# Kernel optimization log

Measured on AMD Instinct MI355X. Metric: run time of the kernel, lower is better.

The kernel has to match this reference:

```python
import jax, jax.numpy as jnp
import numpy as np
from jax import lax

T, N, E, B = 8, 50000, 100000, 512
DN = DE = DG = 128


def _linear_params(key, d_in, d_out):
    k1, k2 = jax.random.split(key)
    s = 1.0 / float(np.sqrt(d_in))
    W = jax.random.uniform(k1, (d_in, d_out), minval=-s, maxval=s, dtype=jnp.float32)
    b = jax.random.uniform(k2, (d_out,), minval=-s, maxval=s, dtype=jnp.float32)
    return W, b


def setup_inputs() -> dict:
    key = jax.random.key(0)
    ks = jax.random.split(key, 12)
    inp = {
        "xs": jax.random.normal(ks[0], (T, N, DN), dtype=jnp.float32),
        "es": jax.random.normal(ks[1], (T, E, DE), dtype=jnp.float32),
        "gs": jax.random.normal(ks[2], (T, B, DG), dtype=jnp.float32),
    }
    i = 3
    for name, d in (("node", DN), ("edge", DE), ("glob", DG)):
        W1, b1 = _linear_params(ks[i], 2 * d, d)  # sig1 sees cat(prev_out, x_t)
        W2, b2 = _linear_params(ks[i + 1], d, d)
        W3, b3 = _linear_params(ks[i + 2], d, d)
        i += 3
        inp[f"W1_{name}"], inp[f"b1_{name}"] = W1, b1
        inp[f"W2_{name}"], inp[f"b2_{name}"] = W2, b2
        inp[f"W3_{name}"], inp[f"b3_{name}"] = W3, b3
    return inp


def _run_component(seq, W1, b1, W2, b2, W3, b3):
    # seq: [T, M, d]; recurrent LSTM-style gating per element, fused in a scan.
    def step(carry, x_t):
        state, out = carry
        forget = jax.nn.sigmoid(jnp.concatenate([out, x_t], axis=-1) @ W1 + b1)
        state = state * forget + jax.nn.sigmoid(x_t @ W2 + b2) * jnp.tanh(x_t)
        out = jnp.tanh(state) * jax.nn.sigmoid(x_t @ W3 + b3)
        return (state, out), None

    (state, out), _ = lax.scan(step, (seq[0], seq[0]), seq)
    return state, out


def reference(xs, es, gs,
              W1_node, b1_node, W2_node, b2_node, W3_node, b3_node,
              W1_edge, b1_edge, W2_edge, b2_edge, W3_edge, b3_edge,
              W1_glob, b1_glob, W2_glob, b2_glob, W3_glob, b3_glob):
    sx, ox = _run_component(xs, W1_node, b1_node, W2_node, b2_node, W3_node, b3_node)
    se, oe = _run_component(es, W1_edge, b1_edge, W2_edge, b2_edge, W3_edge, b3_edge)
    sg, og = _run_component(gs, W1_glob, b1_glob, W2_glob, b2_glob, W3_glob, b3_glob)
    # (state, data) per component: node, edge, glob
    return (sx, se, sg, ox, oe, og)
```

## Files before the change

### kernel.cpp

```cpp
#include <hip/hip_runtime.h>

typedef __attribute__((ext_vector_type(8))) short bf16x8;
typedef __attribute__((ext_vector_type(4))) float f32x4;
typedef __attribute__((ext_vector_type(4))) short s16x4;

__device__ __forceinline__ unsigned cvt_pk(float lo, float hi) {
  unsigned r;
  asm("v_cvt_pk_bf16_f32 %0, %1, %2" : "=v"(r) : "v"(lo), "v"(hi));
  return r;
}
__device__ __forceinline__ float bf2f(short s) {
  return __uint_as_float(((unsigned)(unsigned short)s) << 16);
}
__device__ __forceinline__ float sigm(float z) {
  return __builtin_amdgcn_rcpf(1.f + __builtin_amdgcn_exp2f(-1.44269504089f * z));
}
__device__ __forceinline__ float tanh_(float z) {
  return 1.f - 2.f * __builtin_amdgcn_rcpf(1.f + __builtin_amdgcn_exp2f(2.88539008178f * z));
}

#define WS_MAT 32768
#define WS_COMP 131072
#define NODE_BLOCKS 1563
#define EDGE_BLOCKS 3125
#define GLOB_BLOCKS 16
#define NBLOCKS (NODE_BLOCKS + EDGE_BLOCKS + GLOB_BLOCKS)

#define SWZ(row, byte) ((row) * 256 + ((byte) ^ (((row) & 7) << 4)))
#define BIAS_OFF 40960

__global__ __launch_bounds__(256) void prep_weights(
    const float* __restrict__ W1, const float* __restrict__ W2,
    const float* __restrict__ W3, unsigned char* __restrict__ wsc) {
  const int m = blockIdx.x;
  const float* src; int rowoff = 0;
  if (m == 0)      { src = W1; }
  else if (m == 1) { src = W1; rowoff = 128; }
  else if (m == 2) { src = W2; }
  else             { src = W3; }
  short* dst = (short*)(wsc + (size_t)m * WS_MAT);
  for (int fi = threadIdx.x; fi < 2048; fi += 256) {
    int w = fi >> 8, kc = (fi >> 6) & 3, lane = fi & 63;
    int cc = lane & 15, gg = lane >> 4;
    int wcol = 16 * w + cc;
    int kb = 32 * kc + 8 * gg + rowoff;
    union { bf16x8 h; unsigned u[4]; } v;
#pragma unroll
    for (int j = 0; j < 4; ++j)
      v.u[j] = cvt_pk(src[(size_t)(kb + 2 * j) * 128 + wcol],
                      src[(size_t)(kb + 2 * j + 1) * 128 + wcol]);
    *(bf16x8*)(dst + (size_t)fi * 8) = v.h;
  }
}

__device__ __forceinline__ void pre_tile(
    const char* xb, const float* blds, int row, int g, int w,
    const bf16x8* w1b, const bf16x8* w2, const bf16x8* w3,
    f32x4& u, f32x4& g3, f32x4& aAx) {
  bf16x8 xf[4];
#pragma unroll
  for (int kc = 0; kc < 4; ++kc)
    xf[kc] = *(const bf16x8*)(xb + SWZ(row, 64 * kc + 16 * g));
  s16x4 xe4 = *(const s16x4*)(xb + SWZ(row, 32 * w + 8 * g));
  const int bo = 16 * w + 4 * g;
  f32x4 aX = *(const f32x4*)(blds + bo);
  f32x4 aB = *(const f32x4*)(blds + 128 + bo);
  f32x4 aC = *(const f32x4*)(blds + 256 + bo);
#pragma unroll
  for (int kc = 0; kc < 4; ++kc) {
    aX = __builtin_amdgcn_mfma_f32_16x16x32_bf16(w1b[kc], xf[kc], aX, 0, 0, 0);
    aB = __builtin_amdgcn_mfma_f32_16x16x32_bf16(w2[kc],  xf[kc], aB, 0, 0, 0);
    aC = __builtin_amdgcn_mfma_f32_16x16x32_bf16(w3[kc],  xf[kc], aC, 0, 0, 0);
  }
#pragma unroll
  for (int ri = 0; ri < 4; ++ri) {
    u[ri]  = sigm(aB[ri]) * tanh_(bf2f(xe4[ri]));
    g3[ri] = sigm(aC[ri]);
  }
  aAx = aX;
}

__device__ __forceinline__ void ser_tile(
    const char* ofsrc, char* obw, bool wr, int row, int g, int w,
    const bf16x8* w1a, f32x4 aAx, f32x4 u, f32x4 g3,
    f32x4& st) {
  bf16x8 of[4];
#pragma unroll
  for (int kc = 0; kc < 4; ++kc)
    of[kc] = *(const bf16x8*)(ofsrc + SWZ(row, 64 * kc + 16 * g));
  f32x4 aA = aAx;
#pragma unroll
  for (int kc = 0; kc < 4; ++kc)
    aA = __builtin_amdgcn_mfma_f32_16x16x32_bf16(w1a[kc], of[kc], aA, 0, 0, 0);
  f32x4 ov;
#pragma unroll
  for (int ri = 0; ri < 4; ++ri) {
    float fgt = sigm(aA[ri]);
    st[ri] = st[ri] * fgt + u[ri];
    ov[ri] = tanh_(st[ri]) * g3[ri];
  }
  if (wr) {
    union { s16x4 v; unsigned uu[2]; } ob;
    ob.uu[0] = cvt_pk(ov[0], ov[1]);
    ob.uu[1] = cvt_pk(ov[2], ov[3]);
    *(s16x4*)(obw + SWZ(row, 32 * w + 8 * g)) = ob.v;
  }
}

__global__ __launch_bounds__(512, 2) void glstm(
    const float* __restrict__ xs, const float* __restrict__ es,
    const float* __restrict__ gs, const unsigned char* __restrict__ ws,
    const float* __restrict__ b1n, const float* __restrict__ b2n, const float* __restrict__ b3n,
    const float* __restrict__ b1e, const float* __restrict__ b2e, const float* __restrict__ b3e,
    const float* __restrict__ b1g, const float* __restrict__ b2g, const float* __restrict__ b3g,
    float* __restrict__ dout) {
  __shared__ __align__(16) unsigned char smem[42496];

  const int bid = blockIdx.x, tid = threadIdx.x;
  const float* X; const float *B1, *B2, *B3; float *S, *O; int M, unit, comp;
  if (bid < NODE_BLOCKS) {
    X = xs; M = 50000;  S = dout;              O = dout + 19265536L;
    unit = bid; comp = 0; B1 = b1n; B2 = b2n; B3 = b3n;
  } else if (bid < NODE_BLOCKS + EDGE_BLOCKS) {
    X = es; M = 100000; S = dout + 6400000L;   O = dout + 25665536L;
    unit = bid - NODE_BLOCKS; comp = 1; B1 = b1e; B2 = b2e; B3 = b3e;
  } else {
    X = gs; M = 512;    S = dout + 19200000L;  O = dout + 38465536L;
    unit = bid - (NODE_BLOCKS + EDGE_BLOCKS); comp = 2; B1 = b1g; B2 = b2g; B3 = b3g;
  }

  const int w = tid >> 6, l = tid & 63, c = l & 15, g = l >> 4;
  const int Ra = unit * 32;
  const bool v1 = (Ra + 16) < M;
  const int row0 = c, row1 = 16 + c;

  bf16x8 wA[4][4];
  {
    const short* wsrc = (const short*)(ws + (size_t)comp * WS_COMP);
#pragma unroll
    for (int m = 0; m < 4; ++m)
#pragma unroll
      for (int kc = 0; kc < 4; ++kc)
        wA[m][kc] = *(const bf16x8*)(wsrc + (size_t)m * 16384 + ((w * 4 + kc) * 64 + l) * 8);
  }

  char* xb0 = (char*)smem;
  char* xb1 = (char*)smem + 8192;
  char* xb2 = (char*)smem + 16384;
  char* ob0 = (char*)smem + 24576;
  char* ob1 = (char*)smem + 32768;
  float* blds = (float*)(smem + BIAS_OFF);

  if (tid < 128) {
    blds[tid]       = B1[tid];
    blds[128 + tid] = B2[tid];
    blds[256 + tid] = B3[tid];
  }

  const int srow = tid >> 4;
  const int sbyte = (tid & 15) * 16;
  const int scol = (tid & 15) * 8;
  const bool sv = (Ra + srow) < M;

  if (sv) {
    const float* p0 = X + (size_t)(Ra + srow) * 128 + scol;
    const float* p1 = p0 + (size_t)M * 128;
    f32x4 a0 = *(const f32x4*)p0, a1 = *(const f32x4*)(p0 + 4);
    f32x4 a2 = *(const f32x4*)p1, a3 = *(const f32x4*)(p1 + 4);
    union { bf16x8 h; unsigned u[4]; } o;
    o.u[0] = cvt_pk(a0[0], a0[1]); o.u[1] = cvt_pk(a0[2], a0[3]);
    o.u[2] = cvt_pk(a1[0], a1[1]); o.u[3] = cvt_pk(a1[2], a1[3]);
    *(bf16x8*)(xb0 + SWZ(srow, sbyte)) = o.h;
    o.u[0] = cvt_pk(a2[0], a2[1]); o.u[1] = cvt_pk(a2[2], a2[3]);
    o.u[2] = cvt_pk(a3[0], a3[1]); o.u[3] = cvt_pk(a3[2], a3[3]);
    *(bf16x8*)(xb1 + SWZ(srow, sbyte)) = o.h;
  }
  __syncthreads();

  f32x4 st0, st1;
  {
    s16x4 e0 = *(const s16x4*)(xb0 + SWZ(row0, 32 * w + 8 * g));
    s16x4 e1 = *(const s16x4*)(xb0 + SWZ(row1, 32 * w + 8 * g));
#pragma unroll
    for (int ri = 0; ri < 4; ++ri) { st0[ri] = bf2f(e0[ri]); st1[ri] = bf2f(e1[ri]); }
  }
  f32x4 u0, u1, g30, g31, aAx0, aAx1;
  pre_tile(xb0, blds, row0, g, w, wA[1], wA[2], wA[3], u0, g30, aAx0);
  pre_tile(xb0, blds, row1, g, w, wA[1], wA[2], wA[3], u1, g31, aAx1);

  char* xr = xb1; char* xw = xb2; char* xsp = xb0;
  char* orf = ob0; char* owf = ob1;

#pragma unroll 1
  for (int t = 0; t < 8; ++t) {
    f32x4 pa, pb;
    const bool pf = (t < 6) && sv;
    if (pf) {
      const float* p = X + ((size_t)(t + 2) * M + Ra + srow) * 128 + scol;
      pa = *(const f32x4*)p; pb = *(const f32x4*)(p + 4);
    }

    const char* ofs = (t == 0) ? (const char*)xsp : (const char*)orf;
    const bool wr = (t < 7);
    ser_tile(ofs, owf, wr, row0, g, w, wA[0], aAx0, u0, g30, st0);
    ser_tile(ofs, owf, wr, row1, g, w, wA[0], aAx1, u1, g31, st1);

    if (t < 7) {
      pre_tile(xr, blds, row0, g, w, wA[1], wA[2], wA[3], u0, g30, aAx0);
      pre_tile(xr, blds, row1, g, w, wA[1], wA[2], wA[3], u1, g31, aAx1);
    }

    if (pf) {
      union { bf16x8 h; unsigned u[4]; } o;
      o.u[0] = cvt_pk(pa[0], pa[1]); o.u[1] = cvt_pk(pa[2], pa[3]);
      o.u[2] = cvt_pk(pb[0], pb[1]); o.u[3] = cvt_pk(pb[2], pb[3]);
      *(bf16x8*)(xw + SWZ(srow, sbyte)) = o.h;
    }
    __syncthreads();

    char* tx = xsp; xsp = xr; xr = xw; xw = tx;
    char* to = orf; orf = owf; owf = to;
  }

  {
    f32x4 ov0, ov1;
#pragma unroll
    for (int ri = 0; ri < 4; ++ri) {
      ov0[ri] = tanh_(st0[ri]) * g30[ri];
      ov1[ri] = tanh_(st1[ri]) * g31[ri];
    }
    size_t o0 = (size_t)(Ra + row0) * 128 + 16 * w + 4 * g;
    *(f32x4*)(S + o0) = st0;
    *(f32x4*)(O + o0) = ov0;
    if (v1) {
      size_t o1 = (size_t)(Ra + row1) * 128 + 16 * w + 4 * g;
      *(f32x4*)(S + o1) = st1;
      *(f32x4*)(O + o1) = ov1;
    }
  }
}

extern "C" void kernel_launch(void* const* d_in, const int* in_sizes, int n_in,
                              void* d_out, int out_size, void* d_ws, size_t ws_size,
                              hipStream_t stream) {
  (void)in_sizes; (void)n_in; (void)out_size; (void)ws_size;
  const float* xs = (const float*)d_in[0];
  const float* es = (const float*)d_in[1];
  const float* gs = (const float*)d_in[2];
  unsigned char* ws = (unsigned char*)d_ws;

  for (int comp = 0; comp < 3; ++comp) {
    const float* W1 = (const float*)d_in[3 + comp * 6 + 0];
    const float* W2 = (const float*)d_in[3 + comp * 6 + 2];
    const float* W3 = (const float*)d_in[3 + comp * 6 + 4];
    prep_weights<<<4, 256, 0, stream>>>(W1, W2, W3, ws + (size_t)comp * WS_COMP);
  }
  glstm<<<NBLOCKS, 512, 0, stream>>>(
      xs, es, gs, ws,
      (const float*)d_in[4],  (const float*)d_in[6],  (const float*)d_in[8],
      (const float*)d_in[10], (const float*)d_in[12], (const float*)d_in[14],
      (const float*)d_in[16], (const float*)d_in[18], (const float*)d_in[20],
      (float*)d_out);
}
```

Before: 333.7 us.

## Halve rows per block to 16 and raise occupancy to four blocks per CU

Each block now processes 16 rows instead of 32, so there are twice as many blocks, LDS buffers are halved, and launch bounds ask for four blocks per CU instead of two. Row bounds checks are dropped because every component size divides by 16. The aim is more waves in flight to hide global-load and recurrence latency. In exchange the per-block weight register loads and bias setup are repeated twice as often, each MFMA weight fragment is reused over fewer rows, and the register cap may force spills.

```diff
diff --git a/kernel.cpp b/kernel.cpp
--- a/kernel.cpp
+++ b/kernel.cpp
@@ -21,13 +21,16 @@
 
 #define WS_MAT 32768
 #define WS_COMP 131072
-#define NODE_BLOCKS 1563
-#define EDGE_BLOCKS 3125
-#define GLOB_BLOCKS 16
+#define NODE_BLOCKS 3125
+#define EDGE_BLOCKS 6250
+#define GLOB_BLOCKS 32
 #define NBLOCKS (NODE_BLOCKS + EDGE_BLOCKS + GLOB_BLOCKS)
 
 #define SWZ(row, byte) ((row) * 256 + ((byte) ^ (((row) & 7) << 4)))
-#define BIAS_OFF 40960
+#define XBUF_B 4096
+#define OBUF_B 4096
+#define BIAS_OFF 20480
+#define SMEM_B 22016
 
 __global__ __launch_bounds__(256) void prep_weights(
     const float* __restrict__ W1, const float* __restrict__ W2,
@@ -107,14 +110,14 @@
   }
 }
 
-__global__ __launch_bounds__(512, 2) void glstm(
+__global__ __launch_bounds__(512, 4) void glstm(
     const float* __restrict__ xs, const float* __restrict__ es,
     const float* __restrict__ gs, const unsigned char* __restrict__ ws,
     const float* __restrict__ b1n, const float* __restrict__ b2n, const float* __restrict__ b3n,
     const float* __restrict__ b1e, const float* __restrict__ b2e, const float* __restrict__ b3e,
     const float* __restrict__ b1g, const float* __restrict__ b2g, const float* __restrict__ b3g,
     float* __restrict__ dout) {
-  __shared__ __align__(16) unsigned char smem[42496];
+  __shared__ __align__(16) unsigned char smem[SMEM_B];
 
   const int bid = blockIdx.x, tid = threadIdx.x;
   const float* X; const float *B1, *B2, *B3; float *S, *O; int M, unit, comp;
@@ -130,9 +133,7 @@
   }
 
   const int w = tid >> 6, l = tid & 63, c = l & 15, g = l >> 4;
-  const int Ra = unit * 32;
-  const bool v1 = (Ra + 16) < M;
-  const int row0 = c, row1 = 16 + c;
+  const int Ra = unit * 16;
 
   bf16x8 wA[4][4];
   {
@@ -145,10 +146,10 @@
   }
 
   char* xb0 = (char*)smem;
-  char* xb1 = (char*)smem + 8192;
-  char* xb2 = (char*)smem + 16384;
-  char* ob0 = (char*)smem + 24576;
-  char* ob1 = (char*)smem + 32768;
+  char* xb1 = (char*)smem + XBUF_B;
+  char* xb2 = (char*)smem + 2 * XBUF_B;
+  char* ob0 = (char*)smem + 3 * XBUF_B;
+  char* ob1 = (char*)smem + 3 * XBUF_B + OBUF_B;
   float* blds = (float*)(smem + BIAS_OFF);
 
   if (tid < 128) {
@@ -157,64 +158,54 @@
     blds[256 + tid] = B3[tid];
   }
 
-  const int srow = tid >> 4;
-  const int sbyte = (tid & 15) * 16;
-  const int scol = (tid & 15) * 8;
-  const bool sv = (Ra + srow) < M;
-
-  if (sv) {
+  const int srow = tid >> 5;
+  const int sbyte = (tid & 31) * 8;
+  const int scol = (tid & 31) * 4;
+
+  {
     const float* p0 = X + (size_t)(Ra + srow) * 128 + scol;
     const float* p1 = p0 + (size_t)M * 128;
-    f32x4 a0 = *(const f32x4*)p0, a1 = *(const f32x4*)(p0 + 4);
-    f32x4 a2 = *(const f32x4*)p1, a3 = *(const f32x4*)(p1 + 4);
-    union { bf16x8 h; unsigned u[4]; } o;
+    f32x4 a0 = *(const f32x4*)p0;
+    f32x4 a1 = *(const f32x4*)p1;
+    union { s16x4 v; unsigned u[2]; } o;
     o.u[0] = cvt_pk(a0[0], a0[1]); o.u[1] = cvt_pk(a0[2], a0[3]);
-    o.u[2] = cvt_pk(a1[0], a1[1]); o.u[3] = cvt_pk(a1[2], a1[3]);
-    *(bf16x8*)(xb0 + SWZ(srow, sbyte)) = o.h;
-    o.u[0] = cvt_pk(a2[0], a2[1]); o.u[1] = cvt_pk(a2[2], a2[3]);
-    o.u[2] = cvt_pk(a3[0], a3[1]); o.u[3] = cvt_pk(a3[2], a3[3]);
-    *(bf16x8*)(xb1 + SWZ(srow, sbyte)) = o.h;
+    *(s16x4*)(xb0 + SWZ(srow, sbyte)) = o.v;
+    o.u[0] = cvt_pk(a1[0], a1[1]); o.u[1] = cvt_pk(a1[2], a1[3]);
+    *(s16x4*)(xb1 + SWZ(srow, sbyte)) = o.v;
   }
   __syncthreads();
 
-  f32x4 st0, st1;
-  {
-    s16x4 e0 = *(const s16x4*)(xb0 + SWZ(row0, 32 * w + 8 * g));
-    s16x4 e1 = *(const s16x4*)(xb0 + SWZ(row1, 32 * w + 8 * g));
-#pragma unroll
-    for (int ri = 0; ri < 4; ++ri) { st0[ri] = bf2f(e0[ri]); st1[ri] = bf2f(e1[ri]); }
-  }
-  f32x4 u0, u1, g30, g31, aAx0, aAx1;
-  pre_tile(xb0, blds, row0, g, w, wA[1], wA[2], wA[3], u0, g30, aAx0);
-  pre_tile(xb0, blds, row1, g, w, wA[1], wA[2], wA[3], u1, g31, aAx1);
+  f32x4 st, uu, g3, ax;
+  {
+    s16x4 e = *(const s16x4*)(xb0 + SWZ(c, 32 * w + 8 * g));
+#pragma unroll
+    for (int ri = 0; ri < 4; ++ri) st[ri] = bf2f(e[ri]);
+  }
+  pre_tile(xb0, blds, c, g, w, wA[1], wA[2], wA[3], uu, g3, ax);
 
   char* xr = xb1; char* xw = xb2; char* xsp = xb0;
   char* orf = ob0; char* owf = ob1;
 
 #pragma unroll 1
   for (int t = 0; t < 8; ++t) {
-    f32x4 pa, pb;
-    const bool pf = (t < 6) && sv;
+    f32x4 pa;
+    const bool pf = (t < 6);
     if (pf) {
       const float* p = X + ((size_t)(t + 2) * M + Ra + srow) * 128 + scol;
-      pa = *(const f32x4*)p; pb = *(const f32x4*)(p + 4);
+      pa = *(const f32x4*)p;
     }
 
     const char* ofs = (t == 0) ? (const char*)xsp : (const char*)orf;
     const bool wr = (t < 7);
-    ser_tile(ofs, owf, wr, row0, g, w, wA[0], aAx0, u0, g30, st0);
-    ser_tile(ofs, owf, wr, row1, g, w, wA[0], aAx1, u1, g31, st1);
-
-    if (t < 7) {
-      pre_tile(xr, blds, row0, g, w, wA[1], wA[2], wA[3], u0, g30, aAx0);
-      pre_tile(xr, blds, row1, g, w, wA[1], wA[2], wA[3], u1, g31, aAx1);
-    }
+    ser_tile(ofs, owf, wr, c, g, w, wA[0], ax, uu, g3, st);
+
+    if (t < 7)
+      pre_tile(xr, blds, c, g, w, wA[1], wA[2], wA[3], uu, g3, ax);
 
     if (pf) {
-      union { bf16x8 h; unsigned u[4]; } o;
+      union { s16x4 v; unsigned u[2]; } o;
       o.u[0] = cvt_pk(pa[0], pa[1]); o.u[1] = cvt_pk(pa[2], pa[3]);
-      o.u[2] = cvt_pk(pb[0], pb[1]); o.u[3] = cvt_pk(pb[2], pb[3]);
-      *(bf16x8*)(xw + SWZ(srow, sbyte)) = o.h;
+      *(s16x4*)(xw + SWZ(srow, sbyte)) = o.v;
     }
     __syncthreads();
 
@@ -223,20 +214,12 @@
   }
 
   {
-    f32x4 ov0, ov1;
-#pragma unroll
-    for (int ri = 0; ri < 4; ++ri) {
-      ov0[ri] = tanh_(st0[ri]) * g30[ri];
-      ov1[ri] = tanh_(st1[ri]) * g31[ri];
-    }
-    size_t o0 = (size_t)(Ra + row0) * 128 + 16 * w + 4 * g;
-    *(f32x4*)(S + o0) = st0;
-    *(f32x4*)(O + o0) = ov0;
-    if (v1) {
-      size_t o1 = (size_t)(Ra + row1) * 128 + 16 * w + 4 * g;
-      *(f32x4*)(S + o1) = st1;
-      *(f32x4*)(O + o1) = ov1;
-    }
+    f32x4 ov;
+#pragma unroll
+    for (int ri = 0; ri < 4; ++ri) ov[ri] = tanh_(st[ri]) * g3[ri];
+    size_t o = (size_t)(Ra + c) * 128 + 16 * w + 4 * g;
+    *(f32x4*)(S + o) = st;
+    *(f32x4*)(O + o) = ov;
   }
 }
 
```

Result: faster. 284.9 us (-14.6%).
